# Performance work log

Measured on AMD Instinct MI355X. Metric: run time of the kernel, lower is better.

## Reference

```python
import jax, jax.numpy as jnp
import numpy as np

G, N, E, F, H, O, MO = 64, 2048, 16384, 128, 128, 128, 128


def setup_inputs() -> dict:
    key = jax.random.key(0)
    ks = jax.random.split(key, 12)
    # edges: per-graph contiguous blocks, local indices in [0, N-2] (never touch center N-1)
    src_l = jax.random.randint(ks[0], (G, E), 0, N - 1)
    dst_l = jax.random.randint(ks[1], (G, E), 0, N - 1)
    offs = (jnp.arange(G, dtype=jnp.int64) * N)[:, None]
    edge_index = jnp.stack([(src_l + offs).reshape(-1), (dst_l + offs).reshape(-1)]).astype(jnp.int64)
    x = jax.random.normal(ks[2], (G * N, F), dtype=jnp.float32)
    batch = jnp.repeat(jnp.arange(G, dtype=jnp.int64), N)
    center_node_indices = jnp.full((G,), N - 1, dtype=jnp.int64)
    def lin(k, fan_in, shape):
        return jax.random.normal(k, shape, dtype=jnp.float32) / np.sqrt(fan_in)
    return {
        "x": x, "edge_index": edge_index, "batch": batch,
        "center_node_indices": center_node_indices,
        "W1": lin(ks[3], F, (F, H)), "b1": jnp.zeros((H,), jnp.float32),
        "W2": lin(ks[4], F, (F, O)), "b2": jnp.zeros((O,), jnp.float32),
        "W3": lin(ks[5], F, (F, O)), "b3": jnp.zeros((O,), jnp.float32),
        "Wm": lin(ks[6], H + F, (H + F, MO)), "bm": jnp.zeros((MO,), jnp.float32),
    }


def _gcn(x, src, dst, W, b):
    # PyG GCNConv: D^{-1/2}(A+I)D^{-1/2} X W + b, messages src->dst, deg at dst
    n = x.shape[0]
    h = x @ W
    deg = 1.0 + jax.ops.segment_sum(jnp.ones(src.shape[0], h.dtype), dst, num_segments=n)
    dis = jax.lax.rsqrt(deg)
    msg = h[src] * (dis[src] * dis[dst])[:, None]
    agg = jax.ops.segment_sum(msg, dst, num_segments=n)
    return agg + h * (1.0 / deg)[:, None] + b


_gcn_v = jax.vmap(_gcn, in_axes=(0, 0, 0, None, None))


def reference(x, edge_index, batch, center_node_indices, W1, b1, W2, b2, W3, b3, Wm, bm):
    g = center_node_indices.shape[0]
    n = x.shape[0] // g
    e = edge_index.shape[1] // g
    offs = (jnp.arange(g) * n)[:, None]
    src = edge_index[0].reshape(g, e) - offs  # local per-graph edges
    dst = edge_index[1].reshape(g, e) - offs
    xg = x.reshape(g, n, -1)                      # [G,N,F]
    h1 = _gcn_v(xg, src, dst, W1, b1)             # [G,N,H]
    ce = h1[jnp.arange(g), center_node_indices]   # [G,H] center embeddings
    x_nc = xg[:, : n - 1]                         # non-center nodes (center = N-1)
    hd = W1.shape[1]
    # MLP(cat([center_emb, node_feat])) = relu(ce@Wm_top + x@Wm_bot + bm)
    mask = jax.nn.relu((ce @ Wm[:hd])[:, None, :] + x_nc @ Wm[hd:] + bm)  # [G,N-1,MO]
    core = _gcn_v(mask * x_nc, src, dst, W2, b2)          # [G,N-1,O]
    red = _gcn_v((1.0 - mask) * x_nc, src, dst, W3, b3)   # [G,N-1,O]
    return core.mean(axis=0), red.mean(axis=0)
```

## Files before the change

kernel.cpp:

```cpp
#include <hip/hip_runtime.h>

typedef unsigned short u16;
typedef unsigned int uint32;
typedef __bf16 bf16x8 __attribute__((ext_vector_type(8)));
typedef float f32x4 __attribute__((ext_vector_type(4)));

static constexpr int Gg = 64;
static constexpr int Nn = 2048;
static constexpr int Ee = 16384;
static constexpr int GN = Gg * Nn;
static constexpr int GE = Gg * Ee;

__device__ __forceinline__ u16 f2u(float f) {
    uint32 i = __float_as_uint(f);
    uint32 r = (i + 0x7FFFu + ((i >> 16) & 1u)) >> 16;
    return (u16)r;
}
__device__ __forceinline__ float lo16f(uint32 v) { return __uint_as_float(v << 16); }
__device__ __forceinline__ float hi16f(uint32 v) { return __uint_as_float(v & 0xffff0000u); }


__global__ __launch_bounds__(1024) void k_hist(const int* __restrict__ ei, int* __restrict__ deg,
                                               float* __restrict__ dis, float* __restrict__ invdeg) {
    int g = blockIdx.x, t = threadIdx.x;
    __shared__ int h[2048];
    h[t] = 0; h[t + 1024] = 0;
    __syncthreads();
    #pragma unroll
    for (int k = 0; k < 16; ++k) {
        int d = ei[GE + g * Ee + k * 1024 + t];
        atomicAdd(&h[d & (Nn - 1)], 1);
    }
    __syncthreads();
    #pragma unroll
    for (int k = 0; k < 2; ++k) {
        int i = k * 1024 + t;
        int c = h[i];
        deg[(g << 11) + i] = c;
        float dd = 1.0f + (float)c;
        dis[(g << 11) + i] = rsqrtf(dd);
        invdeg[(g << 11) + i] = 1.0f / dd;
    }
}

__global__ void k_scan_p(const int* __restrict__ deg, int* __restrict__ pos_pn) {
    int p = blockIdx.x, t = threadIdx.x;
    int i0 = 2 * t, i1 = 2 * t + 1;
    int c0 = 0, c1 = 0;
    #pragma unroll
    for (int g8 = 0; g8 < 8; ++g8) {
        int g = p * 8 + g8;
        c0 += deg[(g << 11) + i0];
        c1 += deg[(g << 11) + i1];
    }
    __shared__ int ps[1024];
    ps[t] = c0 + c1; __syncthreads();
    for (int off = 1; off < 1024; off <<= 1) {
        int v = (t >= off) ? ps[t - off] : 0;
        __syncthreads();
        ps[t] += v;
        __syncthreads();
    }
    int base = (p << 17) + ps[t] - (c0 + c1);
    pos_pn[p * 2049 + i0] = base;
    pos_pn[p * 2049 + i1] = base + c0;
    if (t == 1023) pos_pn[p * 2049 + 2048] = (p + 1) << 17;
}

__global__ void k_start(const int* __restrict__ deg, const int* __restrict__ pos_pn,
                        int* __restrict__ gstart) {
    int i = blockIdx.x * 256 + threadIdx.x;
    #pragma unroll
    for (int p = 0; p < 8; ++p) {
        int run = pos_pn[p * 2049 + i];
        #pragma unroll
        for (int g8 = 0; g8 < 8; ++g8) {
            int g = p * 8 + g8;
            gstart[(g << 11) + i] = run;
            run += deg[(g << 11) + i];
        }
    }
}

__global__ __launch_bounds__(1024) void k_scatter(const int* __restrict__ ei, const float* __restrict__ dis,
                                                  const int* __restrict__ gstart, int2* __restrict__ nme) {
    int g = blockIdx.x, t = threadIdx.x;
    __shared__ int curs[2048];
    curs[t] = gstart[(g << 11) + t];
    curs[t + 1024] = gstart[(g << 11) + t + 1024];
    __syncthreads();
    #pragma unroll
    for (int k = 0; k < 16; ++k) {
        int e = g * Ee + k * 1024 + t;
        int s = ei[e];
        int d = ei[GE + e];
        int p = atomicAdd(&curs[d & (Nn - 1)], 1);
        nme[p] = make_int2(s, __float_as_int(dis[s] * dis[d]));
    }
}

__global__ void k_trans(const float* __restrict__ Wm, u16* __restrict__ Wtp) {
    int tid = blockIdx.x * 256 + threadIdx.x;
    int j = tid & 7, l = (tid >> 3) & 63, kc = tid >> 9;
    int ks = kc >> 3, ct = kc & 7, lm = l & 15, lq = l >> 4;
    int f = ks * 32 + lq * 8 + j, c = ct * 16 + lm;
    Wtp[tid] = f2u(Wm[(128 + f) * 128 + c]);
}

__global__ void k_A(const float* __restrict__ x, const int* __restrict__ center,
                    const float* __restrict__ invdeg, const int* __restrict__ gstart,
                    const int* __restrict__ deg, const int2* __restrict__ nme,
                    const float* __restrict__ W1, const float* __restrict__ b1,
                    const float* __restrict__ Wm, const float* __restrict__ bm,
                    float* __restrict__ A) {
    int g = blockIdx.x, t = threadIdx.x;
    __shared__ float cepre[128], ce[128];
    int cg = (g << 11) + center[g];
    float v = x[cg * 128 + t] * invdeg[cg];
    int p0 = gstart[cg], p1 = p0 + deg[cg];
    for (int e = p0; e < p1; ++e) {
        int2 m = nme[e];
        v += __int_as_float(m.y) * x[m.x * 128 + t];
    }
    cepre[t] = v; __syncthreads();
    float a = b1[t];
    #pragma unroll 8
    for (int f = 0; f < 128; ++f) a += cepre[f] * W1[f * 128 + t];
    ce[t] = a; __syncthreads();
    float o = bm[t];
    #pragma unroll 8
    for (int h = 0; h < 128; ++h) o += ce[h] * Wm[h * 128 + t];
    A[g * 128 + t] = o;
}

__global__ __launch_bounds__(256) void k_masky(const float* __restrict__ x,
                                               const u16* __restrict__ Wtp,
                                               const float* __restrict__ A,
                                               u16* __restrict__ xy) {
    __shared__ float sA[128];
    int t = threadIdx.x;
    int tile = blockIdx.x;
    int g = tile >> 5;
    if (t < 128) sA[t] = A[g * 128 + t];
    __syncthreads();

    int w = t >> 6, l = t & 63;
    int lm = l & 15, lq = l >> 4;
    int row = tile * 64 + w * 16 + lm;
    const float* xrow = x + row * 128;
    const bf16x8* Ap = (const bf16x8*)Wtp;

    float4 xf[8];
    #pragma unroll
    for (int ks = 0; ks < 4; ++ks) {
        xf[2 * ks]     = *(const float4*)(xrow + ks * 32 + lq * 8);
        xf[2 * ks + 1] = *(const float4*)(xrow + ks * 32 + lq * 8 + 4);
    }
    union { u16 u[8]; bf16x8 v; } bf[4];
    #pragma unroll
    for (int ks = 0; ks < 4; ++ks) {
        float4 x0 = xf[2 * ks], x1 = xf[2 * ks + 1];
        bf[ks].u[0] = f2u(x0.x); bf[ks].u[1] = f2u(x0.y);
        bf[ks].u[2] = f2u(x0.z); bf[ks].u[3] = f2u(x0.w);
        bf[ks].u[4] = f2u(x1.x); bf[ks].u[5] = f2u(x1.y);
        bf[ks].u[6] = f2u(x1.z); bf[ks].u[7] = f2u(x1.w);
    }

    f32x4 acc[8] = {};
    #pragma unroll
    for (int ks = 0; ks < 4; ++ks) {
        #pragma unroll
        for (int ct = 0; ct < 8; ++ct) {
            bf16x8 a = Ap[(ks * 8 + ct) * 64 + l];
            acc[ct] = __builtin_amdgcn_mfma_f32_16x16x32_bf16(a, bf[ks].v, acc[ct], 0, 0, 0);
        }
    }

    u16* orow = xy + row * 256;
    #pragma unroll
    for (int ct = 0; ct < 8; ++ct) {
        int ch = ct * 16 + lq * 4;
        float4 xv = *(const float4*)(xrow + ch);
        float y0 = fmaxf(acc[ct][0] + sA[ch + 0], 0.f) * xv.x;
        float y1 = fmaxf(acc[ct][1] + sA[ch + 1], 0.f) * xv.y;
        float y2 = fmaxf(acc[ct][2] + sA[ch + 2], 0.f) * xv.z;
        float y3 = fmaxf(acc[ct][3] + sA[ch + 3], 0.f) * xv.w;
        uint4 q;
        q.x = (uint32)f2u(y0)   | ((uint32)f2u(y1)   << 16);
        q.y = (uint32)f2u(xv.x) | ((uint32)f2u(xv.y) << 16);
        q.z = (uint32)f2u(y2)   | ((uint32)f2u(y3)   << 16);
        q.w = (uint32)f2u(xv.z) | ((uint32)f2u(xv.w) << 16);
        *(uint4*)(orow + ct * 32 + lq * 8) = q;
    }
}

#define ACC8(v, cf)                                                     \
    aY0 += (cf) * lo16f((v).x); aY1 += (cf) * hi16f((v).x);             \
    aX0 += (cf) * lo16f((v).y); aX1 += (cf) * hi16f((v).y);             \
    aY2 += (cf) * lo16f((v).z); aY3 += (cf) * hi16f((v).z);             \
    aX2 += (cf) * lo16f((v).w); aX3 += (cf) * hi16f((v).w);

__global__ __launch_bounds__(256) void k_propx(const u16* __restrict__ xy,
                                               const float* __restrict__ invdeg,
                                               const int* __restrict__ pos_pn,
                                               const int2* __restrict__ nme,
                                               float* __restrict__ zp) {
    int b = blockIdx.x;
    int p = b & 7, c = b >> 3;
    int t = threadIdx.x, w = t >> 6, l = t & 63;
    int half = l >> 5, cl = l & 31;
    int i = c * 4 + w;
    float aY0 = 0.f, aY1 = 0.f, aY2 = 0.f, aY3 = 0.f;
    float aX0 = 0.f, aX1 = 0.f, aX2 = 0.f, aX3 = 0.f;

    #pragma unroll
    for (int k = 0; k < 4; ++k) {
        int gid = ((p * 8 + 2 * k + half) << 11) + i;
        float cf = invdeg[gid];
        uint4 v = *(const uint4*)(xy + gid * 256 + cl * 8);
        ACC8(v, cf)
    }

    int j = pos_pn[p * 2049 + i], jend = pos_pn[p * 2049 + i + 1];
    for (; j + 15 < jend; j += 16) {
        int2 m0 = nme[j + half];
        int2 m1 = nme[j + 2 + half];
        int2 m2 = nme[j + 4 + half];
        int2 m3 = nme[j + 6 + half];
        int2 m4 = nme[j + 8 + half];
        int2 m5 = nme[j + 10 + half];
        int2 m6 = nme[j + 12 + half];
        int2 m7 = nme[j + 14 + half];
        uint4 v0 = *(const uint4*)(xy + m0.x * 256 + cl * 8);
        uint4 v1 = *(const uint4*)(xy + m1.x * 256 + cl * 8);
        uint4 v2 = *(const uint4*)(xy + m2.x * 256 + cl * 8);
        uint4 v3 = *(const uint4*)(xy + m3.x * 256 + cl * 8);
        uint4 v4 = *(const uint4*)(xy + m4.x * 256 + cl * 8);
        uint4 v5 = *(const uint4*)(xy + m5.x * 256 + cl * 8);
        uint4 v6 = *(const uint4*)(xy + m6.x * 256 + cl * 8);
        uint4 v7 = *(const uint4*)(xy + m7.x * 256 + cl * 8);
        float c0 = __int_as_float(m0.y), c1 = __int_as_float(m1.y);
        float c2 = __int_as_float(m2.y), c3 = __int_as_float(m3.y);
        float c4 = __int_as_float(m4.y), c5 = __int_as_float(m5.y);
        float c6 = __int_as_float(m6.y), c7 = __int_as_float(m7.y);
        ACC8(v0, c0) ACC8(v1, c1) ACC8(v2, c2) ACC8(v3, c3)
        ACC8(v4, c4) ACC8(v5, c5) ACC8(v6, c6) ACC8(v7, c7)
    }
    for (; j + 7 < jend; j += 8) {
        int2 m0 = nme[j + half];
        int2 m1 = nme[j + 2 + half];
        int2 m2 = nme[j + 4 + half];
        int2 m3 = nme[j + 6 + half];
        uint4 v0 = *(const uint4*)(xy + m0.x * 256 + cl * 8);
        uint4 v1 = *(const uint4*)(xy + m1.x * 256 + cl * 8);
        uint4 v2 = *(const uint4*)(xy + m2.x * 256 + cl * 8);
        uint4 v3 = *(const uint4*)(xy + m3.x * 256 + cl * 8);
        float c0 = __int_as_float(m0.y), c1 = __int_as_float(m1.y);
        float c2 = __int_as_float(m2.y), c3 = __int_as_float(m3.y);
        ACC8(v0, c0) ACC8(v1, c1) ACC8(v2, c2) ACC8(v3, c3)
    }
    for (; j < jend; j += 2) {
        int idx = j + half;
        if (idx < jend) {
            int2 m = nme[idx];
            uint4 v = *(const uint4*)(xy + m.x * 256 + cl * 8);
            float cf = __int_as_float(m.y);
            ACC8(v, cf)
        }
    }

    aY0 += __shfl_xor(aY0, 32, 64); aY1 += __shfl_xor(aY1, 32, 64);
    aX0 += __shfl_xor(aX0, 32, 64); aX1 += __shfl_xor(aX1, 32, 64);
    aY2 += __shfl_xor(aY2, 32, 64); aY3 += __shfl_xor(aY3, 32, 64);
    aX2 += __shfl_xor(aX2, 32, 64); aX3 += __shfl_xor(aX3, 32, 64);
    if (half == 0) {
        float* zr = zp + (((p << 11) + i) << 8) + cl * 8;
        *(float4*)(zr) = make_float4(aY0, aY1, aX0, aX1);
        *(float4*)(zr + 4) = make_float4(aY2, aY3, aX2, aX3);
    }
}

__global__ __launch_bounds__(256) void k_reduce(const float* __restrict__ zp,
                                                const float* __restrict__ W2, const float* __restrict__ b2,
                                                const float* __restrict__ W3, const float* __restrict__ b3,
                                                float* __restrict__ out) {
    int i = blockIdx.x;
    int t = threadIdx.x;
    __shared__ float zm[128], zxm[128];
    float s = 0.f;
    #pragma unroll
    for (int p = 0; p < 8; ++p) s += zp[(((p << 11) + i) << 8) + t];
    s *= (1.0f / 64.0f);
    int k = t >> 2, r = t & 3;
    if (r < 2) zm[2 * k + r] = s; else zxm[2 * k + (r - 2)] = s;
    __syncthreads();
    int cc = t & 127;
    if (t < 128) {
        float acc = b2[cc];
        #pragma unroll 8
        for (int f = 0; f < 128; ++f) acc += zm[f] * W2[f * 128 + cc];
        out[i * 128 + cc] = acc;
    } else {
        float acc = b3[cc];
        #pragma unroll 8
        for (int f = 0; f < 128; ++f) acc += (zxm[f] - zm[f]) * W3[f * 128 + cc];
        out[2047 * 128 + i * 128 + cc] = acc;
    }
}


extern "C" void kernel_launch(void* const* d_in, const int* in_sizes, int n_in,
                              void* d_out, int out_size, void* d_ws, size_t ws_size,
                              hipStream_t stream) {
    const float* x    = (const float*)d_in[0];
    const int* ei     = (const int*)d_in[1];
    const int* center = (const int*)d_in[3];
    const float* W1 = (const float*)d_in[4];
    const float* b1 = (const float*)d_in[5];
    const float* W2 = (const float*)d_in[6];
    const float* b2 = (const float*)d_in[7];
    const float* W3 = (const float*)d_in[8];
    const float* b3 = (const float*)d_in[9];
    const float* Wm = (const float*)d_in[10];
    const float* bm = (const float*)d_in[11];
    float* out = (float*)d_out;

    char* ws = (char*)d_ws;
    int*   degc   = (int*)(ws + 0);
    float* dis    = (float*)(ws + 524288);
    float* invdeg = (float*)(ws + 1048576);
    int*   pos_pn = (int*)(ws + 1572864);
    int*   gstart = (int*)(ws + 1639424);
    float* A      = (float*)(ws + 2163712);
    u16*   Wtp    = (u16*)(ws + 2196480);
    int2*  nme    = (int2*)(ws + 2229248);
    float* zp     = (float*)(ws + 10617856);
    u16*   xy     = (u16*)(ws + 27395072);

    k_hist<<<dim3(Gg), dim3(1024), 0, stream>>>(ei, degc, dis, invdeg);
    k_scan_p<<<dim3(8), dim3(1024), 0, stream>>>(degc, pos_pn);
    k_start<<<dim3(Nn / 256), dim3(256), 0, stream>>>(degc, pos_pn, gstart);
    k_scatter<<<dim3(Gg), dim3(1024), 0, stream>>>(ei, dis, gstart, nme);
    k_trans<<<dim3(64), dim3(256), 0, stream>>>(Wm, Wtp);
    k_A<<<dim3(Gg), dim3(128), 0, stream>>>(x, center, invdeg, gstart, degc, nme, W1, b1, Wm, bm, A);
    k_masky<<<dim3(2048), dim3(256), 0, stream>>>(x, Wtp, A, xy);
    k_propx<<<dim3(4096), dim3(256), 0, stream>>>(xy, invdeg, pos_pn, nme, zp);
    k_reduce<<<dim3(Nn - 1), dim3(256), 0, stream>>>(zp, W2, b2, W3, b3, out);
}
```

Measured before the change: 273.6 us.

## Sub-sort CSR edges by source quarter within each destination bucket

The histogram and scatter now bucket edges by destination and by source range (four quarters of 512 nodes), so each destination's neighbour list is ordered by source block. Start offsets are stored per quarter with packed 16-bit counts. The goal is better locality in the gather in k_propx, where neighbour rows of xy are read roughly in address order. In exchange the setup kernels use four times the shared-memory histogram and more index traffic, and the workspace layout is rearranged so zp overlaps the early buffers.

```diff
diff --git a/kernel.cpp b/kernel.cpp
--- a/kernel.cpp
+++ b/kernel.cpp
@@ -20,38 +20,47 @@
 __device__ __forceinline__ float hi16f(uint32 v) { return __uint_as_float(v & 0xffff0000u); }
 
 
-__global__ __launch_bounds__(1024) void k_hist(const int* __restrict__ ei, int* __restrict__ deg,
+__global__ __launch_bounds__(1024) void k_hist(const int* __restrict__ ei,
+                                               uint32* __restrict__ degq01, uint32* __restrict__ degq23,
                                                float* __restrict__ dis, float* __restrict__ invdeg) {
     int g = blockIdx.x, t = threadIdx.x;
-    __shared__ int h[2048];
-    h[t] = 0; h[t + 1024] = 0;
+    __shared__ int h[8192];
+    #pragma unroll
+    for (int k = 0; k < 8; ++k) h[k * 1024 + t] = 0;
     __syncthreads();
     #pragma unroll
     for (int k = 0; k < 16; ++k) {
-        int d = ei[GE + g * Ee + k * 1024 + t];
-        atomicAdd(&h[d & (Nn - 1)], 1);
+        int e = g * Ee + k * 1024 + t;
+        int s = ei[e] & (Nn - 1);
+        int d = ei[GE + e] & (Nn - 1);
+        atomicAdd(&h[(s >> 9) * 2048 + d], 1);
     }
     __syncthreads();
     #pragma unroll
     for (int k = 0; k < 2; ++k) {
         int i = k * 1024 + t;
-        int c = h[i];
-        deg[(g << 11) + i] = c;
+        int c0 = h[i], c1 = h[2048 + i], c2 = h[4096 + i], c3 = h[6144 + i];
+        int c = c0 + c1 + c2 + c3;
+        degq01[(g << 11) + i] = (uint32)c0 | ((uint32)c1 << 16);
+        degq23[(g << 11) + i] = (uint32)c2 | ((uint32)c3 << 16);
         float dd = 1.0f + (float)c;
         dis[(g << 11) + i] = rsqrtf(dd);
         invdeg[(g << 11) + i] = 1.0f / dd;
     }
 }
 
-__global__ void k_scan_p(const int* __restrict__ deg, int* __restrict__ pos_pn) {
+__global__ void k_scan_p(const uint32* __restrict__ degq01, const uint32* __restrict__ degq23,
+                         int* __restrict__ pos_pn) {
     int p = blockIdx.x, t = threadIdx.x;
     int i0 = 2 * t, i1 = 2 * t + 1;
     int c0 = 0, c1 = 0;
     #pragma unroll
     for (int g8 = 0; g8 < 8; ++g8) {
         int g = p * 8 + g8;
-        c0 += deg[(g << 11) + i0];
-        c1 += deg[(g << 11) + i1];
+        uint32 a01 = degq01[(g << 11) + i0], a23 = degq23[(g << 11) + i0];
+        c0 += (int)((a01 & 0xffff) + (a01 >> 16) + (a23 & 0xffff) + (a23 >> 16));
+        uint32 b01 = degq01[(g << 11) + i1], b23 = degq23[(g << 11) + i1];
+        c1 += (int)((b01 & 0xffff) + (b01 >> 16) + (b23 & 0xffff) + (b23 >> 16));
     }
     __shared__ int ps[1024];
     ps[t] = c0 + c1; __syncthreads();
@@ -67,34 +76,53 @@
     if (t == 1023) pos_pn[p * 2049 + 2048] = (p + 1) << 17;
 }
 
-__global__ void k_start(const int* __restrict__ deg, const int* __restrict__ pos_pn,
-                        int* __restrict__ gstart) {
+__global__ void k_start(const uint32* __restrict__ degq01, const uint32* __restrict__ degq23,
+                        const int* __restrict__ pos_pn, int* __restrict__ gstartq) {
     int i = blockIdx.x * 256 + threadIdx.x;
     #pragma unroll
     for (int p = 0; p < 8; ++p) {
-        int run = pos_pn[p * 2049 + i];
+        uint32 w01[8], w23[8];
         #pragma unroll
         for (int g8 = 0; g8 < 8; ++g8) {
             int g = p * 8 + g8;
-            gstart[(g << 11) + i] = run;
-            run += deg[(g << 11) + i];
+            w01[g8] = degq01[(g << 11) + i];
+            w23[g8] = degq23[(g << 11) + i];
+        }
+        int run = pos_pn[p * 2049 + i];
+        #pragma unroll
+        for (int q = 0; q < 4; ++q) {
+            #pragma unroll
+            for (int g8 = 0; g8 < 8; ++g8) {
+                int g = p * 8 + g8;
+                gstartq[(((g << 11) + i) << 2) + q] = run;
+                int cnt = (q == 0) ? (int)(w01[g8] & 0xffff) :
+                          (q == 1) ? (int)(w01[g8] >> 16) :
+                          (q == 2) ? (int)(w23[g8] & 0xffff) :
+                                     (int)(w23[g8] >> 16);
+                run += cnt;
+            }
         }
     }
 }
 
 __global__ __launch_bounds__(1024) void k_scatter(const int* __restrict__ ei, const float* __restrict__ dis,
-                                                  const int* __restrict__ gstart, int2* __restrict__ nme) {
+                                                  const int* __restrict__ gstartq, int2* __restrict__ nme) {
     int g = blockIdx.x, t = threadIdx.x;
-    __shared__ int curs[2048];
-    curs[t] = gstart[(g << 11) + t];
-    curs[t + 1024] = gstart[(g << 11) + t + 1024];
+    __shared__ int curs[8192];
+    #pragma unroll
+    for (int k = 0; k < 2; ++k) {
+        int d = k * 1024 + t;
+        int4 gs = *(const int4*)&gstartq[((g << 11) + d) << 2];
+        curs[d] = gs.x; curs[2048 + d] = gs.y; curs[4096 + d] = gs.z; curs[6144 + d] = gs.w;
+    }
     __syncthreads();
     #pragma unroll
     for (int k = 0; k < 16; ++k) {
         int e = g * Ee + k * 1024 + t;
         int s = ei[e];
         int d = ei[GE + e];
-        int p = atomicAdd(&curs[d & (Nn - 1)], 1);
+        int q = (s & (Nn - 1)) >> 9;
+        int p = atomicAdd(&curs[q * 2048 + (d & (Nn - 1))], 1);
         nme[p] = make_int2(s, __float_as_int(dis[s] * dis[d]));
     }
 }
@@ -108,8 +136,9 @@
 }
 
 __global__ void k_A(const float* __restrict__ x, const int* __restrict__ center,
-                    const float* __restrict__ invdeg, const int* __restrict__ gstart,
-                    const int* __restrict__ deg, const int2* __restrict__ nme,
+                    const float* __restrict__ invdeg, const int* __restrict__ gstartq,
+                    const uint32* __restrict__ degq01, const uint32* __restrict__ degq23,
+                    const int2* __restrict__ nme,
                     const float* __restrict__ W1, const float* __restrict__ b1,
                     const float* __restrict__ Wm, const float* __restrict__ bm,
                     float* __restrict__ A) {
@@ -117,10 +146,16 @@
     __shared__ float cepre[128], ce[128];
     int cg = (g << 11) + center[g];
     float v = x[cg * 128 + t] * invdeg[cg];
-    int p0 = gstart[cg], p1 = p0 + deg[cg];
-    for (int e = p0; e < p1; ++e) {
-        int2 m = nme[e];
-        v += __int_as_float(m.y) * x[m.x * 128 + t];
+    uint32 a01 = degq01[cg], a23 = degq23[cg];
+    int cnt[4] = { (int)(a01 & 0xffff), (int)(a01 >> 16), (int)(a23 & 0xffff), (int)(a23 >> 16) };
+    int4 gs = *(const int4*)&gstartq[cg << 2];
+    int st[4] = { gs.x, gs.y, gs.z, gs.w };
+    #pragma unroll
+    for (int q = 0; q < 4; ++q) {
+        for (int e = st[q]; e < st[q] + cnt[q]; ++e) {
+            int2 m = nme[e];
+            v += __int_as_float(m.y) * x[m.x * 128 + t];
+        }
     }
     cepre[t] = v; __syncthreads();
     float a = b1[t];
@@ -326,23 +361,24 @@
     float* out = (float*)d_out;
 
     char* ws = (char*)d_ws;
-    int*   degc   = (int*)(ws + 0);
-    float* dis    = (float*)(ws + 524288);
-    float* invdeg = (float*)(ws + 1048576);
-    int*   pos_pn = (int*)(ws + 1572864);
-    int*   gstart = (int*)(ws + 1639424);
-    float* A      = (float*)(ws + 2163712);
-    u16*   Wtp    = (u16*)(ws + 2196480);
-    int2*  nme    = (int2*)(ws + 2229248);
-    float* zp     = (float*)(ws + 10617856);
-    u16*   xy     = (u16*)(ws + 27395072);
-
-    k_hist<<<dim3(Gg), dim3(1024), 0, stream>>>(ei, degc, dis, invdeg);
-    k_scan_p<<<dim3(8), dim3(1024), 0, stream>>>(degc, pos_pn);
-    k_start<<<dim3(Nn / 256), dim3(256), 0, stream>>>(degc, pos_pn, gstart);
-    k_scatter<<<dim3(Gg), dim3(1024), 0, stream>>>(ei, dis, gstart, nme);
+    float*  dis     = (float*)(ws + 0);
+    uint32* degq01  = (uint32*)(ws + 524288);
+    uint32* degq23  = (uint32*)(ws + 1048576);
+    int*    gstartq = (int*)(ws + 1572864);
+    float*  zp      = (float*)(ws + 0);
+    int*    pos_pn  = (int*)(ws + 16777216);
+    float*  invdeg  = (float*)(ws + 16843776);
+    float*  A       = (float*)(ws + 17368064);
+    u16*    Wtp     = (u16*)(ws + 17400832);
+    int2*   nme     = (int2*)(ws + 17433600);
+    u16*    xy      = (u16*)(ws + 25822208);
+
+    k_hist<<<dim3(Gg), dim3(1024), 0, stream>>>(ei, degq01, degq23, dis, invdeg);
+    k_scan_p<<<dim3(8), dim3(1024), 0, stream>>>(degq01, degq23, pos_pn);
+    k_start<<<dim3(Nn / 256), dim3(256), 0, stream>>>(degq01, degq23, pos_pn, gstartq);
+    k_scatter<<<dim3(Gg), dim3(1024), 0, stream>>>(ei, dis, gstartq, nme);
     k_trans<<<dim3(64), dim3(256), 0, stream>>>(Wm, Wtp);
-    k_A<<<dim3(Gg), dim3(128), 0, stream>>>(x, center, invdeg, gstart, degc, nme, W1, b1, Wm, bm, A);
+    k_A<<<dim3(Gg), dim3(128), 0, stream>>>(x, center, invdeg, gstartq, degq01, degq23, nme, W1, b1, Wm, bm, A);
     k_masky<<<dim3(2048), dim3(256), 0, stream>>>(x, Wtp, A, xy);
     k_propx<<<dim3(4096), dim3(256), 0, stream>>>(xy, invdeg, pos_pn, nme, zp);
     k_reduce<<<dim3(Nn - 1), dim3(256), 0, stream>>>(zp, W2, b2, W3, b3, out);
```

Measured after the change: 279.9 us. 2.3% more time.

## Stage per-graph feature slices in LDS for edge propagation, use per-graph CSR

Applied to the files above, without the earlier changes.

The propagation kernel now loads one graph's 16-channel slice of the packed bf16 features into shared memory and resolves neighbor gathers from LDS instead of global memory. It loops over 8 graphs per block and accumulates per node across graphs. The CSR construction drops the cross-graph scan in favor of a per-graph scan, which removes one kernel. The trade-off is only 256 blocks of 512 threads with a large LDS footprint, plus many more nme index reads, since each channel slice re-reads the edge list.

```diff
diff --git a/kernel.cpp b/kernel.cpp
--- a/kernel.cpp
+++ b/kernel.cpp
@@ -43,16 +43,11 @@
     }
 }
 
-__global__ void k_scan_p(const int* __restrict__ deg, int* __restrict__ pos_pn) {
-    int p = blockIdx.x, t = threadIdx.x;
+__global__ __launch_bounds__(1024) void k_scan_g(const int* __restrict__ deg, int* __restrict__ rp) {
+    int g = blockIdx.x, t = threadIdx.x;
     int i0 = 2 * t, i1 = 2 * t + 1;
-    int c0 = 0, c1 = 0;
-    #pragma unroll
-    for (int g8 = 0; g8 < 8; ++g8) {
-        int g = p * 8 + g8;
-        c0 += deg[(g << 11) + i0];
-        c1 += deg[(g << 11) + i1];
-    }
+    int c0 = deg[(g << 11) + i0];
+    int c1 = deg[(g << 11) + i1];
     __shared__ int ps[1024];
     ps[t] = c0 + c1; __syncthreads();
     for (int off = 1; off < 1024; off <<= 1) {
@@ -61,33 +56,17 @@
         ps[t] += v;
         __syncthreads();
     }
-    int base = (p << 17) + ps[t] - (c0 + c1);
-    pos_pn[p * 2049 + i0] = base;
-    pos_pn[p * 2049 + i1] = base + c0;
-    if (t == 1023) pos_pn[p * 2049 + 2048] = (p + 1) << 17;
-}
-
-__global__ void k_start(const int* __restrict__ deg, const int* __restrict__ pos_pn,
-                        int* __restrict__ gstart) {
-    int i = blockIdx.x * 256 + threadIdx.x;
-    #pragma unroll
-    for (int p = 0; p < 8; ++p) {
-        int run = pos_pn[p * 2049 + i];
-        #pragma unroll
-        for (int g8 = 0; g8 < 8; ++g8) {
-            int g = p * 8 + g8;
-            gstart[(g << 11) + i] = run;
-            run += deg[(g << 11) + i];
-        }
-    }
+    int base = g * Ee + ps[t] - (c0 + c1);
+    rp[(g << 11) + i0] = base;
+    rp[(g << 11) + i1] = base + c0;
 }
 
 __global__ __launch_bounds__(1024) void k_scatter(const int* __restrict__ ei, const float* __restrict__ dis,
-                                                  const int* __restrict__ gstart, int2* __restrict__ nme) {
+                                                  const int* __restrict__ rp, int2* __restrict__ nme) {
     int g = blockIdx.x, t = threadIdx.x;
     __shared__ int curs[2048];
-    curs[t] = gstart[(g << 11) + t];
-    curs[t + 1024] = gstart[(g << 11) + t + 1024];
+    curs[t] = rp[(g << 11) + t];
+    curs[t + 1024] = rp[(g << 11) + t + 1024];
     __syncthreads();
     #pragma unroll
     for (int k = 0; k < 16; ++k) {
@@ -108,8 +87,8 @@
 }
 
 __global__ void k_A(const float* __restrict__ x, const int* __restrict__ center,
-                    const float* __restrict__ invdeg, const int* __restrict__ gstart,
-                    const int* __restrict__ deg, const int2* __restrict__ nme,
+                    const float* __restrict__ invdeg, const int* __restrict__ rp,
+                    const int* __restrict__ degc, const int2* __restrict__ nme,
                     const float* __restrict__ W1, const float* __restrict__ b1,
                     const float* __restrict__ Wm, const float* __restrict__ bm,
                     float* __restrict__ A) {
@@ -117,7 +96,7 @@
     __shared__ float cepre[128], ce[128];
     int cg = (g << 11) + center[g];
     float v = x[cg * 128 + t] * invdeg[cg];
-    int p0 = gstart[cg], p1 = p0 + deg[cg];
+    int p0 = rp[cg], p1 = p0 + degc[cg];
     for (int e = p0; e < p1; ++e) {
         int2 m = nme[e];
         v += __int_as_float(m.y) * x[m.x * 128 + t];
@@ -194,89 +173,89 @@
     }
 }
 
-#define ACC8(v, cf)                                                     \
-    aY0 += (cf) * lo16f((v).x); aY1 += (cf) * hi16f((v).x);             \
-    aX0 += (cf) * lo16f((v).y); aX1 += (cf) * hi16f((v).y);             \
-    aY2 += (cf) * lo16f((v).z); aY3 += (cf) * hi16f((v).z);             \
-    aX2 += (cf) * lo16f((v).w); aX3 += (cf) * hi16f((v).w);
-
-__global__ __launch_bounds__(256) void k_propx(const u16* __restrict__ xy,
+#define EACC(d, va, vb, cf)                                              \
+    aY[d][0] += (cf) * lo16f((va).x); aY[d][1] += (cf) * hi16f((va).x);  \
+    aX[d][0] += (cf) * lo16f((va).y); aX[d][1] += (cf) * hi16f((va).y);  \
+    aY[d][2] += (cf) * lo16f((va).z); aY[d][3] += (cf) * hi16f((va).z);  \
+    aX[d][2] += (cf) * lo16f((va).w); aX[d][3] += (cf) * hi16f((va).w);  \
+    aY[d][4] += (cf) * lo16f((vb).x); aY[d][5] += (cf) * hi16f((vb).x);  \
+    aX[d][4] += (cf) * lo16f((vb).y); aX[d][5] += (cf) * hi16f((vb).y);  \
+    aY[d][6] += (cf) * lo16f((vb).z); aY[d][7] += (cf) * hi16f((vb).z);  \
+    aX[d][6] += (cf) * lo16f((vb).w); aX[d][7] += (cf) * hi16f((vb).w);
+
+__global__ __launch_bounds__(512) void k_propx(const u16* __restrict__ xy,
                                                const float* __restrict__ invdeg,
-                                               const int* __restrict__ pos_pn,
+                                               const int* __restrict__ rp,
+                                               const int* __restrict__ degc,
                                                const int2* __restrict__ nme,
                                                float* __restrict__ zp) {
+    __shared__ u16 sx[2 * 2048 * 8];
     int b = blockIdx.x;
-    int p = b & 7, c = b >> 3;
-    int t = threadIdx.x, w = t >> 6, l = t & 63;
-    int half = l >> 5, cl = l & 31;
-    int i = c * 4 + w;
-    float aY0 = 0.f, aY1 = 0.f, aY2 = 0.f, aY3 = 0.f;
-    float aX0 = 0.f, aX1 = 0.f, aX2 = 0.f, aX3 = 0.f;
-
-    #pragma unroll
-    for (int k = 0; k < 4; ++k) {
-        int gid = ((p * 8 + 2 * k + half) << 11) + i;
-        float cf = invdeg[gid];
-        uint4 v = *(const uint4*)(xy + gid * 256 + cl * 8);
-        ACC8(v, cf)
-    }
-
-    int j = pos_pn[p * 2049 + i], jend = pos_pn[p * 2049 + i + 1];
-    for (; j + 15 < jend; j += 16) {
-        int2 m0 = nme[j + half];
-        int2 m1 = nme[j + 2 + half];
-        int2 m2 = nme[j + 4 + half];
-        int2 m3 = nme[j + 6 + half];
-        int2 m4 = nme[j + 8 + half];
-        int2 m5 = nme[j + 10 + half];
-        int2 m6 = nme[j + 12 + half];
-        int2 m7 = nme[j + 14 + half];
-        uint4 v0 = *(const uint4*)(xy + m0.x * 256 + cl * 8);
-        uint4 v1 = *(const uint4*)(xy + m1.x * 256 + cl * 8);
-        uint4 v2 = *(const uint4*)(xy + m2.x * 256 + cl * 8);
-        uint4 v3 = *(const uint4*)(xy + m3.x * 256 + cl * 8);
-        uint4 v4 = *(const uint4*)(xy + m4.x * 256 + cl * 8);
-        uint4 v5 = *(const uint4*)(xy + m5.x * 256 + cl * 8);
-        uint4 v6 = *(const uint4*)(xy + m6.x * 256 + cl * 8);
-        uint4 v7 = *(const uint4*)(xy + m7.x * 256 + cl * 8);
-        float c0 = __int_as_float(m0.y), c1 = __int_as_float(m1.y);
-        float c2 = __int_as_float(m2.y), c3 = __int_as_float(m3.y);
-        float c4 = __int_as_float(m4.y), c5 = __int_as_float(m5.y);
-        float c6 = __int_as_float(m6.y), c7 = __int_as_float(m7.y);
-        ACC8(v0, c0) ACC8(v1, c1) ACC8(v2, c2) ACC8(v3, c3)
-        ACC8(v4, c4) ACC8(v5, c5) ACC8(v6, c6) ACC8(v7, c7)
-    }
-    for (; j + 7 < jend; j += 8) {
-        int2 m0 = nme[j + half];
-        int2 m1 = nme[j + 2 + half];
-        int2 m2 = nme[j + 4 + half];
-        int2 m3 = nme[j + 6 + half];
-        uint4 v0 = *(const uint4*)(xy + m0.x * 256 + cl * 8);
-        uint4 v1 = *(const uint4*)(xy + m1.x * 256 + cl * 8);
-        uint4 v2 = *(const uint4*)(xy + m2.x * 256 + cl * 8);
-        uint4 v3 = *(const uint4*)(xy + m3.x * 256 + cl * 8);
-        float c0 = __int_as_float(m0.y), c1 = __int_as_float(m1.y);
-        float c2 = __int_as_float(m2.y), c3 = __int_as_float(m3.y);
-        ACC8(v0, c0) ACC8(v1, c1) ACC8(v2, c2) ACC8(v3, c3)
-    }
-    for (; j < jend; j += 2) {
-        int idx = j + half;
-        if (idx < jend) {
-            int2 m = nme[idx];
-            uint4 v = *(const uint4*)(xy + m.x * 256 + cl * 8);
-            float cf = __int_as_float(m.y);
-            ACC8(v, cf)
+    int p = b & 7, s = b >> 3;
+    int cc = s & 15, dh = s >> 4;
+    int t = threadIdx.x;
+
+    float aY[2][8] = {}, aX[2][8] = {};
+
+    for (int g8 = 0; g8 < 8; ++g8) {
+        int graph = p * 8 + g8;
+        const u16* gsrc = xy + (size_t)(graph << 11) * 256 + cc * 16;
+        uint4 vst[8];
+        #pragma unroll
+        for (int j = 0; j < 8; ++j) {
+            int idx = j * 512 + t;
+            int r = idx & 2047, k2 = idx >> 11;
+            vst[j] = *(const uint4*)(gsrc + r * 256 + k2 * 8);
         }
-    }
-
-    aY0 += __shfl_xor(aY0, 32, 64); aY1 += __shfl_xor(aY1, 32, 64);
-    aX0 += __shfl_xor(aX0, 32, 64); aX1 += __shfl_xor(aX1, 32, 64);
-    aY2 += __shfl_xor(aY2, 32, 64); aY3 += __shfl_xor(aY3, 32, 64);
-    aX2 += __shfl_xor(aX2, 32, 64); aX3 += __shfl_xor(aX3, 32, 64);
-    if (half == 0) {
-        float* zr = zp + (((p << 11) + i) << 8) + cl * 8;
-        *(float4*)(zr) = make_float4(aY0, aY1, aX0, aX1);
-        *(float4*)(zr + 4) = make_float4(aY2, aY3, aX2, aX3);
+        __syncthreads();
+        #pragma unroll
+        for (int j = 0; j < 8; ++j)
+            *(uint4*)(sx + (j * 512 + t) * 8) = vst[j];
+        __syncthreads();
+
+        int gb = graph << 11;
+        #pragma unroll
+        for (int d = 0; d < 2; ++d) {
+            int i = (dh << 10) + (t << 1) + d;
+            int gid = gb + i;
+            {
+                uint4 va = *(const uint4*)(sx + i * 8);
+                uint4 vb = *(const uint4*)(sx + i * 8 + 16384);
+                float cf = invdeg[gid];
+                EACC(d, va, vb, cf)
+            }
+            int j = rp[gid], jend = j + degc[gid];
+            for (; j + 3 < jend; j += 4) {
+                int2 m0 = nme[j], m1 = nme[j + 1], m2 = nme[j + 2], m3 = nme[j + 3];
+                int s0 = (m0.x & 2047) * 8, s1 = (m1.x & 2047) * 8;
+                int s2 = (m2.x & 2047) * 8, s3 = (m3.x & 2047) * 8;
+                uint4 a0 = *(const uint4*)(sx + s0), b0 = *(const uint4*)(sx + s0 + 16384);
+                uint4 a1 = *(const uint4*)(sx + s1), b1 = *(const uint4*)(sx + s1 + 16384);
+                uint4 a2 = *(const uint4*)(sx + s2), b2 = *(const uint4*)(sx + s2 + 16384);
+                uint4 a3 = *(const uint4*)(sx + s3), b3 = *(const uint4*)(sx + s3 + 16384);
+                float c0 = __int_as_float(m0.y), c1 = __int_as_float(m1.y);
+                float c2 = __int_as_float(m2.y), c3 = __int_as_float(m3.y);
+                EACC(d, a0, b0, c0) EACC(d, a1, b1, c1)
+                EACC(d, a2, b2, c2) EACC(d, a3, b3, c3)
+            }
+            for (; j < jend; ++j) {
+                int2 m = nme[j];
+                int s0 = (m.x & 2047) * 8;
+                uint4 va = *(const uint4*)(sx + s0), vb = *(const uint4*)(sx + s0 + 16384);
+                float cf = __int_as_float(m.y);
+                EACC(d, va, vb, cf)
+            }
+        }
+    }
+
+    #pragma unroll
+    for (int d = 0; d < 2; ++d) {
+        int i = (dh << 10) + (t << 1) + d;
+        float* zr = zp + (size_t)((p << 11) + i) * 256 + cc * 16;
+        *(float4*)(zr)      = make_float4(aY[d][0], aY[d][1], aX[d][0], aX[d][1]);
+        *(float4*)(zr + 4)  = make_float4(aY[d][2], aY[d][3], aX[d][2], aX[d][3]);
+        *(float4*)(zr + 8)  = make_float4(aY[d][4], aY[d][5], aX[d][4], aX[d][5]);
+        *(float4*)(zr + 12) = make_float4(aY[d][6], aY[d][7], aX[d][6], aX[d][7]);
     }
 }
 
@@ -289,7 +268,7 @@
     __shared__ float zm[128], zxm[128];
     float s = 0.f;
     #pragma unroll
-    for (int p = 0; p < 8; ++p) s += zp[(((p << 11) + i) << 8) + t];
+    for (int p = 0; p < 8; ++p) s += zp[(size_t)(((p << 11) + i)) * 256 + t];
     s *= (1.0f / 64.0f);
     int k = t >> 2, r = t & 3;
     if (r < 2) zm[2 * k + r] = s; else zxm[2 * k + (r - 2)] = s;
@@ -329,21 +308,19 @@
     int*   degc   = (int*)(ws + 0);
     float* dis    = (float*)(ws + 524288);
     float* invdeg = (float*)(ws + 1048576);
-    int*   pos_pn = (int*)(ws + 1572864);
-    int*   gstart = (int*)(ws + 1639424);
-    float* A      = (float*)(ws + 2163712);
-    u16*   Wtp    = (u16*)(ws + 2196480);
-    int2*  nme    = (int2*)(ws + 2229248);
-    float* zp     = (float*)(ws + 10617856);
-    u16*   xy     = (u16*)(ws + 27395072);
+    int*   rp     = (int*)(ws + 1572864);
+    float* A      = (float*)(ws + 2097152);
+    u16*   Wtp    = (u16*)(ws + 2129920);
+    int2*  nme    = (int2*)(ws + 2162688);
+    float* zp     = (float*)(ws + 10551296);
+    u16*   xy     = (u16*)(ws + 27328512);
 
     k_hist<<<dim3(Gg), dim3(1024), 0, stream>>>(ei, degc, dis, invdeg);
-    k_scan_p<<<dim3(8), dim3(1024), 0, stream>>>(degc, pos_pn);
-    k_start<<<dim3(Nn / 256), dim3(256), 0, stream>>>(degc, pos_pn, gstart);
-    k_scatter<<<dim3(Gg), dim3(1024), 0, stream>>>(ei, dis, gstart, nme);
+    k_scan_g<<<dim3(Gg), dim3(1024), 0, stream>>>(degc, rp);
+    k_scatter<<<dim3(Gg), dim3(1024), 0, stream>>>(ei, dis, rp, nme);
     k_trans<<<dim3(64), dim3(256), 0, stream>>>(Wm, Wtp);
-    k_A<<<dim3(Gg), dim3(128), 0, stream>>>(x, center, invdeg, gstart, degc, nme, W1, b1, Wm, bm, A);
+    k_A<<<dim3(Gg), dim3(128), 0, stream>>>(x, center, invdeg, rp, degc, nme, W1, b1, Wm, bm, A);
     k_masky<<<dim3(2048), dim3(256), 0, stream>>>(x, Wtp, A, xy);
-    k_propx<<<dim3(4096), dim3(256), 0, stream>>>(xy, invdeg, pos_pn, nme, zp);
+    k_propx<<<dim3(256), dim3(512), 0, stream>>>(xy, invdeg, rp, degc, nme, zp);
     k_reduce<<<dim3(Nn - 1), dim3(256), 0, stream>>>(zp, W2, b2, W3, b3, out);
 }
```

New measurement: 330.0 us. 20.6% more time.
